# Optimization experiments

Hardware: AMD Instinct MI355X
Metric: run time of the kernel (lower is better)

## Reference

```python
import jax, jax.numpy as jnp
import numpy as np
from math import factorial

N_NODES = 10000
N_EDGES = 320000
FEAT = 32
NBASIS = 8
RMAX = 6.0
ZMAX = 119


def _cg(j1, m1, j2, m2, j3, m3):
    if m1 + m2 != m3 or j3 < abs(j1 - j2) or j3 > j1 + j2:
        return 0.0
    f = lambda n: float(factorial(n))
    pre = ((2 * j3 + 1) * f(j1 + j2 - j3) * f(j1 - j2 + j3) * f(-j1 + j2 + j3) / f(j1 + j2 + j3 + 1)) ** 0.5
    pre *= (f(j3 + m3) * f(j3 - m3) * f(j1 - m1) * f(j1 + m1) * f(j2 - m2) * f(j2 + m2)) ** 0.5
    s = 0.0
    for k in range(j1 + j2 + j3 + 1):
        d = [k, j1 + j2 - j3 - k, j1 - m1 - k, j2 + m2 - k, j3 - j2 + m1 + k, j3 - j1 - m2 + k]
        if min(d) < 0:
            continue
        s += (-1) ** k / (f(d[0]) * f(d[1]) * f(d[2]) * f(d[3]) * f(d[4]) * f(d[5]))
    return pre * s


def _u_real(l):
    # complex->real spherical harmonics unitary transform
    U = np.zeros((2 * l + 1, 2 * l + 1), dtype=complex)
    s2 = 1.0 / np.sqrt(2.0)
    for m in range(-l, l + 1):
        i = m + l
        if m == 0:
            U[i, l] = 1.0
        elif m > 0:
            U[i, l + m] = ((-1) ** m) * s2
            U[i, l - m] = s2
        else:
            U[i, l + m] = 1j * s2
            U[i, l - m] = -1j * ((-1) ** m) * s2
    return U


def _real_cg():
    # real Clebsch-Gordan coupling coefficients for l<=2, shape (9,9,9), sparse
    off = [0, 1, 4]
    C = np.zeros((9, 9, 9))
    Us = [_u_real(l) for l in range(3)]
    for l1 in range(3):
        for l2 in range(3):
            for l3 in range(3):
                if l3 < abs(l1 - l2) or l3 > l1 + l2:
                    continue
                cg = np.zeros((2 * l1 + 1, 2 * l2 + 1, 2 * l3 + 1))
                for m1 in range(-l1, l1 + 1):
                    for m2 in range(-l2, l2 + 1):
                        m3 = m1 + m2
                        if abs(m3) <= l3:
                            cg[m1 + l1, m2 + l2, m3 + l3] = _cg(l1, m1, l2, m2, l3, m3)
                blk = np.einsum('ia,jb,kc,abc->ijk', Us[l1], Us[l2], np.conj(Us[l3]), cg.astype(complex))
                C[off[l1]:off[l1] + 2 * l1 + 1, off[l2]:off[l2] + 2 * l2 + 1, off[l3]:off[l3] + 2 * l3 + 1] = blk.real + blk.imag
    return C

CGC = jnp.asarray(_real_cg(), dtype=jnp.float32)
SL = [slice(0, 1), slice(1, 4), slice(4, 9)]
PATHS0 = [(0, 0, 0), (0, 1, 1), (0, 2, 2)]
PATHS1 = [(l1, l2, l3) for l1 in range(3) for l2 in range(3) for l3 in range(3) if abs(l1 - l2) <= l3 <= l1 + l2]
PATHS2 = [(0, 0, 0), (1, 1, 0), (2, 2, 0)]


def _real_sph(u):
    x, y, z = u[:, 0], u[:, 1], u[:, 2]
    c0 = 0.28209479177387814
    c1 = 0.4886025119029199
    c2a = 1.0925484305920792
    c2b = 0.31539156525252005
    c2c = 0.5462742152960396
    return jnp.stack([c0 * jnp.ones_like(x), c1 * y, c1 * z, c1 * x,
                      c2a * x * y, c2a * y * z, c2b * (3.0 * z * z - 1.0), c2a * x * z,
                      c2c * (x * x - y * y)], axis=-1)


def _message_pass(x, rad, Y, src, dst, W, paths, out_dim, n_nodes):
    # gather src node features -> per-edge CG tensor product with (radial x Ylm) basis -> scatter-add to dst
    xs = x[src, 0]  # (E, Dx, F)
    msg = jnp.zeros((rad.shape[0], out_dim, x.shape[-1]), x.dtype)
    for p, (l1, l2, l3) in enumerate(paths):
        w = rad @ W[p]  # (E, F) learned radial path weights
        contrib = jnp.einsum('abc,eaf,eb,ef->ecf', CGC[SL[l1], SL[l2], SL[l3]], xs[:, SL[l1], :], Y[:, SL[l2]], w)
        msg = msg.at[:, SL[l3], :].add(contrib)
    y = jax.ops.segment_sum(msg, dst, num_segments=n_nodes)
    return y[:, None]  # (N, 1, out_dim, F)


def _eadd(a, b):
    if a.shape[2] == b.shape[2]:
        return a + b
    if a.shape[2] < b.shape[2]:
        a, b = b, a
    return a.at[:, :, :b.shape[2], :].add(b)


def _edense(x, K, b):
    # equivariant Dense: shared kernel across degrees, bias only on scalar (l=0) channel
    y = jnp.einsum('npdf,fg->npdg', x, K)
    return y.at[:, :, 0, :].add(b)


def _esilu(x):
    # silu on scalars, sigmoid(scalar)-gated scaling on l>0 components (equivariant)
    if x.shape[2] == 1:
        return jax.nn.silu(x)
    s = x[:, :, 0:1, :]
    return jnp.concatenate([jax.nn.silu(s), x[:, :, 1:, :] * jax.nn.sigmoid(s)], axis=2)


def _forward(dr_vec, Z, neighbor_idxs, embed, wmp0, wmp1, wmp2, dk1, db1, dk2, db2):
    idx_i, idx_j = neighbor_idxs[0], neighbor_idxs[1]
    nN = Z.shape[0]
    r = jnp.sqrt(jnp.sum(dr_vec * dr_vec, axis=-1) + 1e-12)  # (E,)
    u = dr_vec / r[:, None]
    n = jnp.arange(1, NBASIS + 1, dtype=dr_vec.dtype)
    rad = jnp.sqrt(2.0 / RMAX) * jnp.sin(n * jnp.pi * r[:, None] / RMAX) / r[:, None]  # Bessel radial basis
    t = jnp.clip(r / RMAX, 0.0, 1.0 - 1e-6)
    cut = jnp.where(r < RMAX, jnp.exp(1.0 - 1.0 / (1.0 - t * t)), 0.0)  # smooth cutoff
    mask = (idx_i != idx_j).astype(dr_vec.dtype)  # mask padding/self edges
    rad = rad * (cut * mask)[:, None]
    Y = _real_sph(u)  # (E, 9)
    x = embed[Z][:, None, None, :]  # (N, 1, 1, F)
    for it, (paths, W) in enumerate([(PATHS0, wmp0), (PATHS1, wmp1), (PATHS2, wmp2)]):
        last = it == 2
        y = _message_pass(x, rad, Y, idx_j, idx_i, W, paths, 1 if last else 9, nN)
        if last:
            x = x[:, :, 0:1, :]  # change_max_degree_or_type -> scalars only
        y = _eadd(x, y)
        y = _edense(y, dk1[it], db1[it])
        y = _esilu(y)
        y = _edense(y, dk2[it], db2[it])
        x = _eadd(x, y)
    return x[:, 0, 0, :]


def setup_inputs():
    key = jax.random.key(0)
    ks = jax.random.split(key, 10)
    dr_vec = 2.0 * jax.random.normal(ks[0], (N_EDGES, 3), jnp.float32)
    Z = jax.random.randint(ks[1], (N_NODES,), 0, ZMAX)
    neighbor_idxs = jax.random.randint(ks[2], (2, N_EDGES), 0, N_NODES)
    embed = jax.random.normal(ks[3], (ZMAX, FEAT), jnp.float32)
    sB = 1.0 / np.sqrt(NBASIS)
    wmp0 = sB * jax.random.normal(ks[4], (len(PATHS0), NBASIS, FEAT), jnp.float32)
    wmp1 = sB * jax.random.normal(ks[5], (len(PATHS1), NBASIS, FEAT), jnp.float32)
    wmp2 = sB * jax.random.normal(ks[6], (len(PATHS2), NBASIS, FEAT), jnp.float32)
    sF = 1.0 / np.sqrt(FEAT)
    dense_k1 = sF * jax.random.normal(ks[7], (3, FEAT, FEAT), jnp.float32)
    dense_b1 = jnp.zeros((3, FEAT), jnp.float32)
    dense_k2 = 0.1 * sF * jax.random.normal(ks[8], (3, FEAT, FEAT), jnp.float32)
    dense_b2 = jnp.zeros((3, FEAT), jnp.float32)
    return {"dr_vec": dr_vec, "Z": Z, "neighbor_idxs": neighbor_idxs, "embed": embed,
            "wmp0": wmp0, "wmp1": wmp1, "wmp2": wmp2,
            "dense_k1": dense_k1, "dense_b1": dense_b1, "dense_k2": dense_k2, "dense_b2": dense_b2}


def reference(dr_vec, Z, neighbor_idxs, embed, wmp0, wmp1, wmp2, dense_k1, dense_b1, dense_k2, dense_b2):
    return _forward(dr_vec, Z, neighbor_idxs, embed, wmp0, wmp1, wmp2, dense_k1, dense_b1, dense_k2, dense_b2)
```

## Files before the change

kernel.cpp:

```cpp
#include <hip/hip_runtime.h>
#include <type_traits>
#include <cstdint>
#include <cstddef>

#define N_FEAT 32
#define NBASIS 8
#define SPAN   16
#define BSLOTS 8
#define BEDGES (SPAN*BSLOTS)

namespace cgc {

constexpr double dfact(int n){ double r=1.0; for(int i=2;i<=n;++i) r*=(double)i; return r; }

constexpr double dsqrt(double x){
  if(x<=0.0) return 0.0;
  double g = x>1.0 ? x : 1.0;
  for(int i=0;i<200;++i){ double ng = 0.5*(g + x/g); if(ng==g) break; g=ng; }
  return g;
}

constexpr double cg1(int j1,int m1,int j2,int m2,int j3,int m3){
  int adiff = j1-j2; if(adiff<0) adiff=-adiff;
  if(m1+m2!=m3 || j3<adiff || j3>j1+j2) return 0.0;
  double pre = dsqrt((double)(2*j3+1)*dfact(j1+j2-j3)*dfact(j1-j2+j3)*dfact(-j1+j2+j3)/dfact(j1+j2+j3+1));
  pre = pre*dsqrt(dfact(j3+m3)*dfact(j3-m3)*dfact(j1-m1)*dfact(j1+m1)*dfact(j2-m2)*dfact(j2+m2));
  double s=0.0;
  for(int k=0;k<=j1+j2+j3;++k){
    int d1=j1+j2-j3-k, d2=j1-m1-k, d3=j2+m2-k, d4=j3-j2+m1+k, d5=j3-j1-m2+k;
    if(d1<0||d2<0||d3<0||d4<0||d5<0) continue;
    double term = 1.0/(dfact(k)*dfact(d1)*dfact(d2)*dfact(d3)*dfact(d4)*dfact(d5));
    s += (k&1)? -term : term;
  }
  return pre*s;
}

struct Tab { float v[9][9][9]; };

constexpr Tab make(){
  Tab T{};
  int off[3]={0,1,4};
  double Ure[3][5][5]={}, Uim[3][5][5]={};
  const double s2 = dsqrt(0.5);
  for(int l=0;l<3;++l){
    for(int m=-l;m<=l;++m){
      int i=m+l;
      if(m==0){ Ure[l][i][l]=1.0; }
      else if(m>0){
        Ure[l][i][l+m] = ((m&1)? -1.0:1.0)*s2;
        Ure[l][i][l-m] = s2;
      } else {
        int am=-m;
        Uim[l][i][l+m] = s2;
        Uim[l][i][l-m] = -(((am&1)?-1.0:1.0))*s2;
      }
    }
  }
  for(int l1=0;l1<3;++l1) for(int l2=0;l2<3;++l2) for(int l3=0;l3<3;++l3){
    int lo = l1-l2; if(lo<0) lo=-lo;
    if(l3<lo || l3>l1+l2) continue;
    int d1=2*l1+1, d2=2*l2+1, d3=2*l3+1;
    double cg[5][5][5]={};
    for(int m1=-l1;m1<=l1;++m1) for(int m2=-l2;m2<=l2;++m2){
      int m3=m1+m2;
      if(m3>=-l3 && m3<=l3) cg[m1+l1][m2+l2][m3+l3] = cg1(l1,m1,l2,m2,l3,m3);
    }
    double t1re[5][5][5]={}, t1im[5][5][5]={};
    for(int a=0;a<d1;++a) for(int b=0;b<d2;++b) for(int k=0;k<d3;++k){
      double sre=0, sim=0;
      for(int c=0;c<d3;++c){
        double g=cg[a][b][c]; if(g==0.0) continue;
        sre += g*Ure[l3][k][c];
        sim -= g*Uim[l3][k][c];
      }
      t1re[a][b][k]=sre; t1im[a][b][k]=sim;
    }
    double t2re[5][5][5]={}, t2im[5][5][5]={};
    for(int a=0;a<d1;++a) for(int j=0;j<d2;++j) for(int k=0;k<d3;++k){
      double sre=0,sim=0;
      for(int b=0;b<d2;++b){
        double ur=Ure[l2][j][b], ui=Uim[l2][j][b];
        if(ur==0.0&&ui==0.0) continue;
        sre += ur*t1re[a][b][k]-ui*t1im[a][b][k];
        sim += ur*t1im[a][b][k]+ui*t1re[a][b][k];
      }
      t2re[a][j][k]=sre; t2im[a][j][k]=sim;
    }
    for(int i=0;i<d1;++i) for(int j=0;j<d2;++j) for(int k=0;k<d3;++k){
      double sre=0,sim=0;
      for(int a=0;a<d1;++a){
        double ur=Ure[l1][i][a], ui=Uim[l1][i][a];
        if(ur==0.0&&ui==0.0) continue;
        sre += ur*t2re[a][j][k]-ui*t2im[a][j][k];
        sim += ur*t2im[a][j][k]+ui*t2re[a][j][k];
      }
      T.v[off[l1]+i][off[l2]+j][off[l3]+k] = (float)(sre+sim);
    }
  }
  return T;
}

constexpr Tab T = make();

}

template<int I, int N, typename F>
__device__ __forceinline__ void sfor(F&& f){
  if constexpr (I < N){
    f(std::integral_constant<int,I>{});
    sfor<I+1,N>(static_cast<F&&>(f));
  }
}

constexpr int LOFF[3] = {0,1,4};

struct PS0 {
  static constexpr int NP=3;
  static constexpr int L[3][3]={{0,0,0},{0,1,1},{0,2,2}};
  static constexpr int ALO=0, AHI=1, OD=9, WOFF=0;
  static constexpr int MINW=4;
};
struct PS1a {
  static constexpr int NP=9;
  static constexpr int L[9][3]={{0,0,0},{0,1,1},{0,2,2},
                                {1,0,1},{1,1,0},{1,1,1},{1,1,2},{1,2,1},{1,2,2}};
  static constexpr int ALO=0, AHI=4, OD=9, WOFF=0;
  static constexpr int MINW=3;
};
struct PS1b {
  static constexpr int NP=6;
  static constexpr int L[6][3]={{2,0,2},{2,1,1},{2,1,2},{2,2,0},{2,2,1},{2,2,2}};
  static constexpr int ALO=4, AHI=9, OD=9, WOFF=9*NBASIS*N_FEAT;
  static constexpr int MINW=3;
};
struct PS2 {
  static constexpr int NP=3;
  static constexpr int L[3][3]={{0,0,0},{1,1,0},{2,2,0}};
  static constexpr int ALO=0, AHI=9, OD=1, WOFF=0;
  static constexpr int MINW=3;
};

__global__ void zero_kernel(int* __restrict__ a, int n){
  int i = blockIdx.x*256 + threadIdx.x;
  if(i<n) a[i]=0;
}

__global__ void count_kernel(const int* __restrict__ dst, int* __restrict__ cnt, int E){
  int e = blockIdx.x*256 + threadIdx.x;
  if(e<E) atomicAdd(&cnt[dst[e]], 1);
}

__global__ void __launch_bounds__(1024) scan_kernel(const int* __restrict__ cnt,
                                                    int* __restrict__ row_ptr,
                                                    int* __restrict__ cursor, int n){
  __shared__ int part[1024];
  const int tid = threadIdx.x;
  const int chunk = (n + 1023) >> 10;
  const int s0 = tid*chunk;
  const int s1 = (s0+chunk < n) ? s0+chunk : n;
  int s=0;
  for(int i=s0;i<s1;++i) s += cnt[i];
  part[tid]=s; __syncthreads();
  for(int off=1; off<1024; off<<=1){
    int v = 0;
    if(tid>=off) v = part[tid-off];
    __syncthreads();
    part[tid] += v;
    __syncthreads();
  }
  int run = part[tid] - s;
  for(int i=s0;i<s1;++i){
    int cv = cnt[i];
    row_ptr[i]=run; cursor[i]=run;
    run += cv;
  }
  if(tid==1023) row_ptr[n] = part[1023];
}

__global__ void fill_kernel(const int* __restrict__ dst, const int* __restrict__ src,
                            int* __restrict__ cursor, int* __restrict__ perm,
                            int* __restrict__ srcs, int* __restrict__ dsts, int E){
  int e = blockIdx.x*256 + threadIdx.x;
  if(e<E){
    int d = dst[e];
    int pos = atomicAdd(&cursor[d], 1);
    perm[e] = pos;
    srcs[pos] = src[e];
    dsts[pos] = d;
  }
}

__global__ void geom_kernel(const float* __restrict__ dr, const int* __restrict__ ii,
                            const int* __restrict__ jj, const int* __restrict__ perm,
                            float* __restrict__ radY, int E){
  int e = blockIdx.x*256 + threadIdx.x;
  if(e>=E) return;
  float dx=dr[3*e], dy=dr[3*e+1], dz=dr[3*e+2];
  float r2 = fmaf(dx,dx,fmaf(dy,dy,fmaf(dz,dz,1e-12f)));
  float r = sqrtf(r2);
  float inv = 1.f/r;
  float ux=dx*inv, uy=dy*inv, uz=dz*inv;
  float t = r*(1.f/6.f);
  t = fminf(fmaxf(t,0.f), 1.f-1e-6f);
  float cut = 0.f;
  if (r < 6.f) cut = expf(1.f - 1.f/(1.f - t*t));
  if (ii[e]==jj[e]) cut = 0.f;
  float base = 0.57735026918962576f * inv * cut;
  float* o = radY + (size_t)perm[e]*20;
  const float pir = 0.52359877559829887f * r;
  #pragma unroll
  for(int nb=1; nb<=8; ++nb) o[nb-1] = base * sinf((float)nb * pir);
  o[8]  = 0.28209479177387814f;
  o[9]  = 0.4886025119029199f*uy;
  o[10] = 0.4886025119029199f*uz;
  o[11] = 0.4886025119029199f*ux;
  o[12] = 1.0925484305920792f*ux*uy;
  o[13] = 1.0925484305920792f*uy*uz;
  o[14] = 0.31539156525252005f*(3.f*uz*uz-1.f);
  o[15] = 1.0925484305920792f*ux*uz;
  o[16] = 0.5462742152960396f*(ux*ux-uy*uy);
  o[17]=0.f; o[18]=0.f; o[19]=0.f;
}

__global__ void init_kernel(const float* __restrict__ embed, const int* __restrict__ Z,
                            float* __restrict__ xA, int nN){
  int i = blockIdx.x*256 + threadIdx.x;
  if(i >= nN*N_FEAT) return;
  int n = i>>5, f = i&31;
  xA[(size_t)n*288 + f] = embed[Z[n]*N_FEAT + f];
}

template<class PS>
__global__ void __launch_bounds__(256, PS::MINW) mp_kernel(
    const int* __restrict__ dsts, const int* __restrict__ srcs,
    const float* __restrict__ radY, const float* __restrict__ x_in,
    const float* __restrict__ W, float* __restrict__ ymsg, int E)
{
  constexpr int NP = PS::NP;
  constexpr int ALO = PS::ALO, AHI = PS::AHI, DA = AHI-ALO;
  constexpr int OD = PS::OD;

  __shared__ float sRad[BEDGES*20];
  __shared__ int   sSrc[BEDGES];
  __shared__ int   sDst[BEDGES];

  const int tid  = threadIdx.x;
  const int base = blockIdx.x * BEDGES;
  const int nE   = (base + BEDGES <= E) ? BEDGES : (E - base);

  {
    const float4* g4 = (const float4*)(radY + (size_t)base*20);
    float4* s4 = (float4*)sRad;
    const int n4 = nE*5;
    for (int i=tid; i<n4; i+=256) s4[i] = g4[i];
    for (int i=tid; i<nE;  i+=256){ sSrc[i]=srcs[base+i]; sDst[i]=dsts[base+i]; }
  }
  __syncthreads();

  const int f  = tid & 31;
  int k        = (tid>>5)*SPAN;
  const int k1 = (k+SPAN < nE) ? k+SPAN : nE;
  if (k >= nE) return;

  float Wreg[NP][NBASIS];
  sfor<0,NP>([&](auto P){
    sfor<0,NBASIS>([&](auto Q){
      Wreg[P.value][Q.value] = W[PS::WOFF + (P.value*NBASIS+Q.value)*N_FEAT + f];
    });
  });

  float msg[OD];
  sfor<0,OD>([&](auto C){ msg[C.value]=0.f; });

  int d = sDst[k];
  float xsA[DA];
  {
    const float* xb = x_in + (size_t)sSrc[k]*288 + ALO*N_FEAT + f;
    sfor<0,DA>([&](auto A){ xsA[A.value] = xb[A.value*N_FEAT]; });
  }

  for (;;){
    const int kn = k + 1;
    const bool more = kn < k1;
    float xsB[DA]; int dn = -1;
    if (more){
      const float* xb = x_in + (size_t)sSrc[kn]*288 + ALO*N_FEAT + f;
      sfor<0,DA>([&](auto A){ xsB[A.value] = xb[A.value*N_FEAT]; });
      dn = sDst[kn];
    }

    const float* rp = sRad + k*20;
    const float4 q0 = *(const float4*)(rp);
    const float4 q1 = *(const float4*)(rp+4);
    const float4 q2 = *(const float4*)(rp+8);
    const float4 q3 = *(const float4*)(rp+12);
    const float y8 = rp[16];
    const float rad[8] = {q0.x,q0.y,q0.z,q0.w,q1.x,q1.y,q1.z,q1.w};
    const float Yv[9]  = {q2.x,q2.y,q2.z,q2.w,q3.x,q3.y,q3.z,q3.w,y8};

    sfor<0,NP>([&](auto P){
      constexpr int p  = P.value;
      constexpr int l1 = PS::L[p][0], l2 = PS::L[p][1], l3 = PS::L[p][2];
      constexpr int o1 = LOFF[l1], o2 = LOFF[l2], o3 = LOFF[l3];
      float w = 0.f;
      sfor<0,NBASIS>([&](auto Q){ w = fmaf(rad[Q.value], Wreg[p][Q.value], w); });
      sfor<0,2*l2+1>([&](auto B){
        constexpr int b = B.value;
        const float yw = Yv[o2+b]*w;
        sfor<0,2*l1+1>([&](auto A){
          constexpr int a = A.value;
          sfor<0,2*l3+1>([&](auto C){
            constexpr int c = C.value;
            constexpr float cgv = cgc::T.v[o1+a][o2+b][o3+c];
            if constexpr (cgv > 1e-7f || cgv < -1e-7f){
              msg[o3+c] = fmaf(cgv*xsA[o1+a-ALO], yw, msg[o3+c]);
            }
          });
        });
      });
    });

    if (dn != d){
      float* yb = ymsg + ((size_t)d*OD)*N_FEAT + f;
      sfor<0,OD>([&](auto C){
        atomicAdd(yb + C.value*N_FEAT, msg[C.value]);
        msg[C.value] = 0.f;
      });
      d = dn;
    }
    if (!more) break;

    sfor<0,DA>([&](auto A){ xsA[A.value] = xsB[A.value]; });
    k = kn;
  }
}

template<int DX>
__global__ void __launch_bounds__(256) nodeA_kernel(
    const float* __restrict__ xin, const float* __restrict__ ymsg,
    const float* __restrict__ K1, const float* __restrict__ b1,
    const float* __restrict__ K2, const float* __restrict__ b2,
    float* __restrict__ xout, int nN)
{
  __shared__ float sK1[1024], sK2[1024], sb1[32], sb2[32];
  __shared__ float tb[8][9][32];
  const int tid = threadIdx.x;
  for(int i=tid;i<1024;i+=256){ sK1[i]=K1[i]; sK2[i]=K2[i]; }
  if(tid<32){ sb1[tid]=b1[tid]; sb2[tid]=b2[tid]; }
  __syncthreads();
  const int h = tid>>5, f = tid&31;
  const int n = blockIdx.x*8 + h;
  const bool valid = n < nN;
  const int nc = valid ? n : 0;
  float xi[9];
  #pragma unroll
  for(int c=0;c<9;++c){
    float t = ymsg[((size_t)nc*9+c)*32+f];
    float x = 0.f;
    if (c<DX) x = xin[((size_t)nc*9+c)*32+f];
    xi[c]=x;
    tb[h][c][f] = t + x;
  }
  __syncthreads();
  float u[9];
  #pragma unroll
  for(int c=0;c<9;++c){
    float acc = (c==0) ? sb1[f] : 0.f;
    #pragma unroll
    for(int g=0;g<32;++g) acc = fmaf(tb[h][c][g], sK1[g*32+f], acc);
    u[c]=acc;
  }
  const float gate = 1.f/(1.f+expf(-u[0]));
  __syncthreads();
  #pragma unroll
  for(int c=0;c<9;++c) tb[h][c][f] = u[c]*gate;
  __syncthreads();
  #pragma unroll
  for(int c=0;c<9;++c){
    float acc = (c==0) ? sb2[f] : 0.f;
    #pragma unroll
    for(int g=0;g<32;++g) acc = fmaf(tb[h][c][g], sK2[g*32+f], acc);
    if (valid) xout[((size_t)n*9+c)*32+f] = acc + ((c<DX) ? xi[c] : 0.f);
  }
}

__global__ void __launch_bounds__(256) nodeB_kernel(
    const float* __restrict__ xin, const float* __restrict__ msg0,
    const float* __restrict__ K1, const float* __restrict__ b1,
    const float* __restrict__ K2, const float* __restrict__ b2,
    float* __restrict__ out, int nN)
{
  __shared__ float sK1[1024], sK2[1024], sb1[32], sb2[32];
  __shared__ float tb[8][32];
  const int tid = threadIdx.x;
  for(int i=tid;i<1024;i+=256){ sK1[i]=K1[i]; sK2[i]=K2[i]; }
  if(tid<32){ sb1[tid]=b1[tid]; sb2[tid]=b2[tid]; }
  __syncthreads();
  const int h = tid>>5, f = tid&31;
  const int n = blockIdx.x*8 + h;
  const bool valid = n < nN;
  const int nc = valid ? n : 0;
  const float x0 = xin[(size_t)nc*288 + f];
  tb[h][f] = msg0[(size_t)nc*32+f] + x0;
  __syncthreads();
  float acc = sb1[f];
  #pragma unroll
  for(int g=0;g<32;++g) acc = fmaf(tb[h][g], sK1[g*32+f], acc);
  const float gate = 1.f/(1.f+expf(-acc));
  const float v = acc*gate;
  __syncthreads();
  tb[h][f] = v;
  __syncthreads();
  float acc2 = sb2[f];
  #pragma unroll
  for(int g=0;g<32;++g) acc2 = fmaf(tb[h][g], sK2[g*32+f], acc2);
  if (valid) out[(size_t)n*32+f] = x0 + acc2;
}

extern "C" void kernel_launch(void* const* d_in, const int* in_sizes, int n_in,
                              void* d_out, int out_size, void* d_ws, size_t ws_size,
                              hipStream_t stream) {
  const float* dr    = (const float*)d_in[0];
  const int*   Z     = (const int*)  d_in[1];
  const int*   nbr   = (const int*)  d_in[2];
  const float* embed = (const float*)d_in[3];
  const float* wmp0  = (const float*)d_in[4];
  const float* wmp1  = (const float*)d_in[5];
  const float* wmp2  = (const float*)d_in[6];
  const float* dk1   = (const float*)d_in[7];
  const float* db1   = (const float*)d_in[8];
  const float* dk2   = (const float*)d_in[9];
  const float* db2   = (const float*)d_in[10];
  const int nN = in_sizes[1];
  const int E  = in_sizes[2]/2;
  const int* idx_i = nbr;
  const int* idx_j = nbr + E;

  uintptr_t base = (uintptr_t)d_ws;
  auto alloc = [&](size_t bytes)->void*{
    uintptr_t p = (base + 255) & ~(uintptr_t)255;
    base = p + bytes;
    return (void*)p;
  };
  float* radY    = (float*)alloc((size_t)E*20*4);
  int*   cnt     = (int*)  alloc((size_t)nN*4);
  int*   cursor  = (int*)  alloc((size_t)nN*4);
  int*   row_ptr = (int*)  alloc((size_t)(nN+1)*4);
  int*   perm    = (int*)  alloc((size_t)E*4);
  int*   srcs    = (int*)  alloc((size_t)E*4);
  int*   dsts    = (int*)  alloc((size_t)E*4);
  float* xA      = (float*)alloc((size_t)nN*288*4);
  float* xB      = (float*)alloc((size_t)nN*288*4);
  float* ymsg    = (float*)alloc((size_t)nN*288*4);

  const int gE = (E+255)/256;
  const int gN = (nN+255)/256;

  zero_kernel <<<gN, 256, 0, stream>>>(cnt, nN);
  count_kernel<<<gE, 256, 0, stream>>>(idx_i, cnt, E);
  scan_kernel <<<1, 1024, 0, stream>>>(cnt, row_ptr, cursor, nN);
  fill_kernel <<<gE, 256, 0, stream>>>(idx_i, idx_j, cursor, perm, srcs, dsts, E);

  geom_kernel <<<gE, 256, 0, stream>>>(dr, idx_i, idx_j, perm, radY, E);
  init_kernel <<<(nN*N_FEAT+255)/256, 256, 0, stream>>>(embed, Z, xA, nN);

  const int gND = (nN+7)/8;
  const int gMP = (E + BEDGES - 1) / BEDGES;
  const size_t ymsgBytes = (size_t)nN*288*4;

  hipMemsetAsync(ymsg, 0, ymsgBytes, stream);
  mp_kernel<PS0><<<gMP, 256, 0, stream>>>(dsts, srcs, radY, xA, wmp0, ymsg, E);
  nodeA_kernel<1><<<gND, 256, 0, stream>>>(xA, ymsg, dk1, db1, dk2, db2, xB, nN);
  hipMemsetAsync(ymsg, 0, ymsgBytes, stream);
  mp_kernel<PS1a><<<gMP, 256, 0, stream>>>(dsts, srcs, radY, xB, wmp1, ymsg, E);
  mp_kernel<PS1b><<<gMP, 256, 0, stream>>>(dsts, srcs, radY, xB, wmp1, ymsg, E);
  nodeA_kernel<9><<<gND, 256, 0, stream>>>(xB, ymsg, dk1+1024, db1+32, dk2+1024, db2+32, xA, nN);
  hipMemsetAsync(ymsg, 0, (size_t)nN*32*4, stream);
  mp_kernel<PS2><<<gMP, 256, 0, stream>>>(dsts, srcs, radY, xA, wmp2, ymsg, E);
  nodeB_kernel<<<gND, 256, 0, stream>>>(xA, ymsg, dk1+2048, db1+64, dk2+2048, db2+64,
                                        (float*)d_out, nN);
}
```

Baseline: 434.2 us.

## Interleave node features per channel for vectorized gathers, pack src/dst, widen edge span

Node feature storage changes from channel-major [n][9][32] to feature-major [n][32][12] (padded), so each lane's gather of the irreps channels for a source node becomes one or two float4 loads instead of strided scalar loads. Source and destination indices are packed into a single int2 array, which cuts the index loads in the message-passing kernel. The edges per warp (SPAN) double from 16 to 32, giving fewer blocks and longer accumulation runs per destination. The cost is that node kernels now read and write with a 48-byte stride per lane, which is uncoalesced, and the padded layout uses more memory.

```diff
diff --git a/kernel.cpp b/kernel.cpp
--- a/kernel.cpp
+++ b/kernel.cpp
@@ -5,7 +5,8 @@
 
 #define N_FEAT 32
 #define NBASIS 8
-#define SPAN   16
+#define XCH    12
+#define SPAN   32
 #define BSLOTS 8
 #define BEDGES (SPAN*BSLOTS)
 
@@ -179,14 +180,13 @@
 
 __global__ void fill_kernel(const int* __restrict__ dst, const int* __restrict__ src,
                             int* __restrict__ cursor, int* __restrict__ perm,
-                            int* __restrict__ srcs, int* __restrict__ dsts, int E){
+                            int2* __restrict__ sd, int E){
   int e = blockIdx.x*256 + threadIdx.x;
   if(e<E){
     int d = dst[e];
     int pos = atomicAdd(&cursor[d], 1);
     perm[e] = pos;
-    srcs[pos] = src[e];
-    dsts[pos] = d;
+    sd[pos] = make_int2(src[e], d);
   }
 }
 
@@ -227,22 +227,21 @@
   int i = blockIdx.x*256 + threadIdx.x;
   if(i >= nN*N_FEAT) return;
   int n = i>>5, f = i&31;
-  xA[(size_t)n*288 + f] = embed[Z[n]*N_FEAT + f];
+  xA[((size_t)n*N_FEAT + f)*XCH] = embed[Z[n]*N_FEAT + f];
 }
 
 template<class PS>
 __global__ void __launch_bounds__(256, PS::MINW) mp_kernel(
-    const int* __restrict__ dsts, const int* __restrict__ srcs,
-    const float* __restrict__ radY, const float* __restrict__ x_in,
-    const float* __restrict__ W, float* __restrict__ ymsg, int E)
+    const int2* __restrict__ sd, const float* __restrict__ radY,
+    const float* __restrict__ x_in, const float* __restrict__ W,
+    float* __restrict__ ymsg, int E)
 {
   constexpr int NP = PS::NP;
   constexpr int ALO = PS::ALO, AHI = PS::AHI, DA = AHI-ALO;
   constexpr int OD = PS::OD;
 
   __shared__ float sRad[BEDGES*20];
-  __shared__ int   sSrc[BEDGES];
-  __shared__ int   sDst[BEDGES];
+  __shared__ int2  sSD[BEDGES];
 
   const int tid  = threadIdx.x;
   const int base = blockIdx.x * BEDGES;
@@ -253,14 +252,14 @@
     float4* s4 = (float4*)sRad;
     const int n4 = nE*5;
     for (int i=tid; i<n4; i+=256) s4[i] = g4[i];
-    for (int i=tid; i<nE;  i+=256){ sSrc[i]=srcs[base+i]; sDst[i]=dsts[base+i]; }
+    for (int i=tid; i<nE;  i+=256) sSD[i] = sd[base+i];
   }
   __syncthreads();
 
   const int f  = tid & 31;
-  int k        = (tid>>5)*SPAN;
-  const int k1 = (k+SPAN < nE) ? k+SPAN : nE;
-  if (k >= nE) return;
+  const int k0 = (tid>>5)*SPAN;
+  const int k1 = (k0+SPAN < nE) ? k0+SPAN : nE;
+  if (k0 >= nE) return;
 
   float Wreg[NP][NBASIS];
   sfor<0,NP>([&](auto P){
@@ -269,24 +268,42 @@
     });
   });
 
+  auto gather = [&](float (&xs)[DA], int src){
+    const float* xb = x_in + ((size_t)src*N_FEAT + f)*XCH + ALO;
+    if constexpr (DA == 1){
+      xs[0] = xb[0];
+    } else if constexpr (DA == 4){
+      const float4 v = *(const float4*)xb;
+      xs[0]=v.x; xs[1]=v.y; xs[2]=v.z; xs[3]=v.w;
+    } else if constexpr (DA == 5){
+      const float4 v = *(const float4*)xb;
+      xs[0]=v.x; xs[1]=v.y; xs[2]=v.z; xs[3]=v.w;
+      xs[4]=xb[4];
+    } else {
+      const float4 v0 = *(const float4*)xb;
+      const float4 v1 = *(const float4*)(xb+4);
+      xs[0]=v0.x; xs[1]=v0.y; xs[2]=v0.z; xs[3]=v0.w;
+      xs[4]=v1.x; xs[5]=v1.y; xs[6]=v1.z; xs[7]=v1.w;
+      xs[8]=xb[8];
+    }
+  };
+
   float msg[OD];
   sfor<0,OD>([&](auto C){ msg[C.value]=0.f; });
 
-  int d = sDst[k];
+  int2 sd0 = sSD[k0];
+  int d = sd0.y;
   float xsA[DA];
-  {
-    const float* xb = x_in + (size_t)sSrc[k]*288 + ALO*N_FEAT + f;
-    sfor<0,DA>([&](auto A){ xsA[A.value] = xb[A.value*N_FEAT]; });
-  }
-
-  for (;;){
+  gather(xsA, sd0.x);
+
+  for (int k = k0;;){
     const int kn = k + 1;
     const bool more = kn < k1;
     float xsB[DA]; int dn = -1;
     if (more){
-      const float* xb = x_in + (size_t)sSrc[kn]*288 + ALO*N_FEAT + f;
-      sfor<0,DA>([&](auto A){ xsB[A.value] = xb[A.value*N_FEAT]; });
-      dn = sDst[kn];
+      const int2 sdn = sSD[kn];
+      gather(xsB, sdn.x);
+      dn = sdn.y;
     }
 
     const float* rp = sRad + k*20;
@@ -352,12 +369,13 @@
   const int n = blockIdx.x*8 + h;
   const bool valid = n < nN;
   const int nc = valid ? n : 0;
+  const float* xrow = xin + ((size_t)nc*N_FEAT + f)*XCH;
   float xi[9];
   #pragma unroll
   for(int c=0;c<9;++c){
     float t = ymsg[((size_t)nc*9+c)*32+f];
     float x = 0.f;
-    if (c<DX) x = xin[((size_t)nc*9+c)*32+f];
+    if (c<DX) x = xrow[c];
     xi[c]=x;
     tb[h][c][f] = t + x;
   }
@@ -375,12 +393,13 @@
   #pragma unroll
   for(int c=0;c<9;++c) tb[h][c][f] = u[c]*gate;
   __syncthreads();
+  float* orow = xout + ((size_t)n*N_FEAT + f)*XCH;
   #pragma unroll
   for(int c=0;c<9;++c){
     float acc = (c==0) ? sb2[f] : 0.f;
     #pragma unroll
     for(int g=0;g<32;++g) acc = fmaf(tb[h][c][g], sK2[g*32+f], acc);
-    if (valid) xout[((size_t)n*9+c)*32+f] = acc + ((c<DX) ? xi[c] : 0.f);
+    if (valid) orow[c] = acc + ((c<DX) ? xi[c] : 0.f);
   }
 }
 
@@ -400,7 +419,7 @@
   const int n = blockIdx.x*8 + h;
   const bool valid = n < nN;
   const int nc = valid ? n : 0;
-  const float x0 = xin[(size_t)nc*288 + f];
+  const float x0 = xin[((size_t)nc*N_FEAT + f)*XCH];
   tb[h][f] = msg0[(size_t)nc*32+f] + x0;
   __syncthreads();
   float acc = sb1[f];
@@ -447,10 +466,9 @@
   int*   cursor  = (int*)  alloc((size_t)nN*4);
   int*   row_ptr = (int*)  alloc((size_t)(nN+1)*4);
   int*   perm    = (int*)  alloc((size_t)E*4);
-  int*   srcs    = (int*)  alloc((size_t)E*4);
-  int*   dsts    = (int*)  alloc((size_t)E*4);
-  float* xA      = (float*)alloc((size_t)nN*288*4);
-  float* xB      = (float*)alloc((size_t)nN*288*4);
+  int2*  sd      = (int2*) alloc((size_t)E*8);
+  float* xA      = (float*)alloc((size_t)nN*N_FEAT*XCH*4);
+  float* xB      = (float*)alloc((size_t)nN*N_FEAT*XCH*4);
   float* ymsg    = (float*)alloc((size_t)nN*288*4);
 
   const int gE = (E+255)/256;
@@ -459,7 +477,7 @@
   zero_kernel <<<gN, 256, 0, stream>>>(cnt, nN);
   count_kernel<<<gE, 256, 0, stream>>>(idx_i, cnt, E);
   scan_kernel <<<1, 1024, 0, stream>>>(cnt, row_ptr, cursor, nN);
-  fill_kernel <<<gE, 256, 0, stream>>>(idx_i, idx_j, cursor, perm, srcs, dsts, E);
+  fill_kernel <<<gE, 256, 0, stream>>>(idx_i, idx_j, cursor, perm, sd, E);
 
   geom_kernel <<<gE, 256, 0, stream>>>(dr, idx_i, idx_j, perm, radY, E);
   init_kernel <<<(nN*N_FEAT+255)/256, 256, 0, stream>>>(embed, Z, xA, nN);
@@ -469,14 +487,14 @@
   const size_t ymsgBytes = (size_t)nN*288*4;
 
   hipMemsetAsync(ymsg, 0, ymsgBytes, stream);
-  mp_kernel<PS0><<<gMP, 256, 0, stream>>>(dsts, srcs, radY, xA, wmp0, ymsg, E);
+  mp_kernel<PS0><<<gMP, 256, 0, stream>>>(sd, radY, xA, wmp0, ymsg, E);
   nodeA_kernel<1><<<gND, 256, 0, stream>>>(xA, ymsg, dk1, db1, dk2, db2, xB, nN);
   hipMemsetAsync(ymsg, 0, ymsgBytes, stream);
-  mp_kernel<PS1a><<<gMP, 256, 0, stream>>>(dsts, srcs, radY, xB, wmp1, ymsg, E);
-  mp_kernel<PS1b><<<gMP, 256, 0, stream>>>(dsts, srcs, radY, xB, wmp1, ymsg, E);
+  mp_kernel<PS1a><<<gMP, 256, 0, stream>>>(sd, radY, xB, wmp1, ymsg, E);
+  mp_kernel<PS1b><<<gMP, 256, 0, stream>>>(sd, radY, xB, wmp1, ymsg, E);
   nodeA_kernel<9><<<gND, 256, 0, stream>>>(xB, ymsg, dk1+1024, db1+32, dk2+1024, db2+32, xA, nN);
   hipMemsetAsync(ymsg, 0, (size_t)nN*32*4, stream);
-  mp_kernel<PS2><<<gMP, 256, 0, stream>>>(dsts, srcs, radY, xA, wmp2, ymsg, E);
+  mp_kernel<PS2><<<gMP, 256, 0, stream>>>(sd, radY, xA, wmp2, ymsg, E);
   nodeB_kernel<<<gND, 256, 0, stream>>>(xA, ymsg, dk1+2048, db1+64, dk2+2048, db2+64,
                                         (float*)d_out, nN);
 }
```

New measurement: 472.6 us. +8.8%, slower.
